# Optimization experiments

Measured on AMD Instinct MI355X. Metric: run time of the kernel, lower is better.

Reference implementation:

```python
import jax, jax.numpy as jnp
import numpy as np

# BERT-base dims
B, S = 32, 512
L, H, DH, DB, DFF, V = 12, 12, 64, 768, 3072, 30522
# Mamba2 dims
DM = 512            # d_model
DST = 128           # d_state
P = 64              # headdim
DI = 1024           # d_inner = expand * d_model
NH = DI // P        # 16 mamba heads
DCONV = 4
CONV_DIM = DI + 2 * DST
DIP = 2 * DI + 2 * DST + NH   # in_proj output width
ED = 256            # final embed_dim


def setup_inputs():
    keys = iter(jax.random.split(jax.random.key(0), 64))
    def nrm(shape, s=0.02):
        return jax.random.normal(next(keys), shape, jnp.float32) * s
    return {
        "input_ids": jax.random.randint(next(keys), (B, S), 0, V, jnp.int32),
        "attention_mask": jnp.ones((B, S), jnp.int32),
        # frozen BERT params (layer dims stacked on axis 0)
        "tok_emb": nrm((V, DB)), "pos_emb": nrm((S, DB)), "type_emb": nrm((2, DB)),
        "emb_ln_g": jnp.ones((DB,)), "emb_ln_b": jnp.zeros((DB,)),
        "Wq": nrm((L, DB, DB)), "bq": jnp.zeros((L, DB)),
        "Wk": nrm((L, DB, DB)), "bk": jnp.zeros((L, DB)),
        "Wv": nrm((L, DB, DB)), "bv": jnp.zeros((L, DB)),
        "Wo": nrm((L, DB, DB)), "bo": jnp.zeros((L, DB)),
        "ln1_g": jnp.ones((L, DB)), "ln1_b": jnp.zeros((L, DB)),
        "Wf1": nrm((L, DB, DFF)), "bf1": jnp.zeros((L, DFF)),
        "Wf2": nrm((L, DFF, DB)), "bf2": jnp.zeros((L, DB)),
        "ln2_g": jnp.ones((L, DB)), "ln2_b": jnp.zeros((L, DB)),
        # trainable head params
        "W_pb": nrm((DB, DM)), "b_pb": jnp.zeros((DM,)),
        "W_in": nrm((DM, DIP)),
        "conv_w": nrm((CONV_DIM, DCONV), 0.2), "conv_b": jnp.zeros((CONV_DIM,)),
        "dt_bias": nrm((NH,), 0.5),
        "A_log": jnp.log(jnp.arange(1, NH + 1, dtype=jnp.float32)),
        "Dskip": jnp.ones((NH,)),
        "norm_g": jnp.ones((DI,)),
        "W_out": nrm((DI, DM)),
        "W_proj": nrm((DM, ED)), "b_proj": jnp.zeros((ED,)),
    }


def _layernorm(x, g, b, eps=1e-12):
    m = x.mean(-1, keepdims=True)
    v = ((x - m) ** 2).mean(-1, keepdims=True)
    return (x - m) * jax.lax.rsqrt(v + eps) * g + b


def _bert(input_ids, attention_mask, p):
    x = p["tok_emb"][input_ids] + p["pos_emb"][None] + p["type_emb"][0]
    x = _layernorm(x, p["emb_ln_g"], p["emb_ln_b"])
    bias = jnp.where(attention_mask[:, None, None, :] > 0, 0.0, -1e9)  # [B,1,1,S]
    inv_sqrt_dh = 1.0 / np.sqrt(DH).astype(np.float32)

    def layer(x, w):
        Wq, bq, Wk, bk, Wv, bv, Wo, bo, g1, b1, W1, c1, W2, c2, g2, b2 = w
        q = (x @ Wq + bq).reshape(B, S, H, DH)
        k = (x @ Wk + bk).reshape(B, S, H, DH)
        v = (x @ Wv + bv).reshape(B, S, H, DH)
        sc = jnp.einsum("bqhd,bkhd->bhqk", q, k) * inv_sqrt_dh + bias
        a = jax.nn.softmax(sc, axis=-1)
        o = jnp.einsum("bhqk,bkhd->bqhd", a, v).reshape(B, S, DB) @ Wo + bo
        x = _layernorm(x + o, g1, b1)
        f = jax.nn.gelu(x @ W1 + c1) @ W2 + c2
        x = _layernorm(x + f, g2, b2)
        return x, None

    stacked = (p["Wq"], p["bq"], p["Wk"], p["bk"], p["Wv"], p["bv"], p["Wo"], p["bo"],
               p["ln1_g"], p["ln1_b"], p["Wf1"], p["bf1"], p["Wf2"], p["bf2"],
               p["ln2_g"], p["ln2_b"])
    x, _ = jax.lax.scan(layer, x, stacked)
    return x


def _mamba_head(bert_out, p):
    xm = bert_out @ p["W_pb"] + p["b_pb"]                       # [B,S,DM]
    zxbcdt = xm @ p["W_in"]                                     # [B,S,DIP]
    z = zxbcdt[..., :DI]
    xBC = zxbcdt[..., DI:DI + CONV_DIM]
    dt = jax.nn.softplus(zxbcdt[..., DI + CONV_DIM:] + p["dt_bias"])  # [B,S,NH]
    # causal depthwise conv1d (kernel DCONV) + silu
    xc = jax.lax.conv_general_dilated(
        xBC.transpose(0, 2, 1), p["conv_w"][:, None, :], (1,), [(DCONV - 1, 0)],
        dimension_numbers=("NCH", "OIH", "NCH"), feature_group_count=CONV_DIM)
    xBC = jax.nn.silu((xc + p["conv_b"][:, None]).transpose(0, 2, 1))
    xs = xBC[..., :DI].reshape(B, S, NH, P)
    Bm = xBC[..., DI:DI + DST]                                  # [B,S,N] (ngroups=1)
    Cm = xBC[..., DI + DST:]                                    # [B,S,N]
    A = -jnp.exp(p["A_log"])                                    # [NH]
    dA = jnp.exp(dt * A)                                        # [B,S,NH]
    dtx = dt[..., None] * xs                                    # [B,S,NH,P]

    def step(h, ins):                                           # h: [B,NH,P,N]
        dA_t, dtx_t, B_t, C_t = ins
        h = dA_t[:, :, None, None] * h + dtx_t[..., None] * B_t[:, None, None, :]
        y = jnp.einsum("bhpn,bn->bhp", h, C_t)
        return h, y

    h0 = jnp.zeros((B, NH, P, DST))
    _, y = jax.lax.scan(step, h0, (dA.transpose(1, 0, 2), dtx.transpose(1, 0, 2, 3),
                                   Bm.transpose(1, 0, 2), Cm.transpose(1, 0, 2)))
    y = y.transpose(1, 0, 2, 3) + p["Dskip"][None, None, :, None] * xs  # [B,S,NH,P]
    # gated RMSNorm: rmsnorm(y * silu(z)) * g
    y = y.reshape(B, S, DI) * jax.nn.silu(z)
    y = y * jax.lax.rsqrt((y * y).mean(-1, keepdims=True) + 1e-5) * p["norm_g"]
    out = y @ p["W_out"]                                        # [B,S,DM]
    pooled = out.mean(axis=1)                                   # [B,DM]
    return pooled @ p["W_proj"] + p["b_proj"]                   # [B,ED]


def reference(input_ids, attention_mask, tok_emb, pos_emb, type_emb, emb_ln_g, emb_ln_b,
              Wq, bq, Wk, bk, Wv, bv, Wo, bo, ln1_g, ln1_b, Wf1, bf1, Wf2, bf2, ln2_g, ln2_b,
              W_pb, b_pb, W_in, conv_w, conv_b, dt_bias, A_log, Dskip, norm_g, W_out,
              W_proj, b_proj):
    p = dict(locals())
    bert_out = _bert(input_ids, attention_mask, p)
    return _mamba_head(bert_out, p)
```

## Files before the change

### kernel.cpp

```cpp
#include <hip/hip_runtime.h>
#include <hip/hip_bf16.h>


typedef __attribute__((ext_vector_type(4))) float f32x4;
typedef __attribute__((ext_vector_type(4))) short s16x4;
typedef __attribute__((ext_vector_type(8))) short s16x8;

#define DEV __device__ __forceinline__

DEV short f2bf(float f) {
  union { float f; unsigned u; } x; x.f = f;
  unsigned r = x.u + 0x7fffu + ((x.u >> 16) & 1u);
  return (short)(r >> 16);
}
DEV float bf2f(short h) {
  union { unsigned u; float f; } x; x.u = ((unsigned)(unsigned short)h) << 16;
  return x.f;
}
DEV float gelu_f(float x) {
  float u = 0.7978845608028654f * (x + 0.044715f * x * x * x);
  return 0.5f * x * (1.f + tanhf(u));
}
DEV float silu_f(float x) { return x / (1.f + __expf(-x)); }

DEV void glds16(const short* g, short* l) {
  __builtin_amdgcn_global_load_lds(
      (const __attribute__((address_space(1))) void*)g,
      (__attribute__((address_space(3))) void*)l, 16, 0, 0);
}
DEV void glds16f(const float* g, float* l) {
  __builtin_amdgcn_global_load_lds(
      (const __attribute__((address_space(1))) void*)g,
      (__attribute__((address_space(3))) void*)l, 16, 0, 0);
}
DEV void glds4f(const float* g, float* l) {
  __builtin_amdgcn_global_load_lds(
      (const __attribute__((address_space(1))) void*)g,
      (__attribute__((address_space(3))) void*)l, 4, 0, 0);
}

DEV float block_reduce_sum_256(float v, float* red) {
  #pragma unroll
  for (int o = 1; o < 64; o <<= 1) v += __shfl_xor(v, o);
  __syncthreads();
  if ((threadIdx.x & 63) == 0) red[threadIdx.x >> 6] = v;
  __syncthreads();
  return red[0] + red[1] + red[2] + red[3];
}

DEV float wave_reduce_sum(float v) {
  #pragma unroll
  for (int o = 1; o < 64; o <<= 1) v += __shfl_xor(v, o);
  return v;
}

__global__ __launch_bounds__(256) void transconv4_all_kernel(
    const float* __restrict__ Wq, const float* __restrict__ Wk,
    const float* __restrict__ Wv, const float* __restrict__ Wo,
    short* __restrict__ Wall)
{
  int l = blockIdx.z >> 2, which = blockIdx.z & 3;
  const float* Wb = (which == 0) ? Wq : (which == 1) ? Wk : (which == 2) ? Wv : Wo;
  const float* W = Wb + (size_t)l * 589824;
  short* Wtz = Wall + (size_t)l * 7077888 + (size_t)which * 589824;
  __shared__ float tile[32][33];
  int tx = threadIdx.x & 31, ty = threadIdx.x >> 5;
  int n0 = blockIdx.x * 32, k0 = blockIdx.y * 32;
  #pragma unroll
  for (int i = 0; i < 4; i++)
    tile[ty + i * 8][tx] = W[(size_t)(k0 + ty + i * 8) * 768 + n0 + tx];
  __syncthreads();
  #pragma unroll
  for (int i = 0; i < 4; i++)
    Wtz[(size_t)(n0 + ty + i * 8) * 768 + k0 + tx] = f2bf(tile[tx][ty + i * 8]);
}

__global__ __launch_bounds__(256) void transconv_f1_all_kernel(
    const float* __restrict__ Wf1, short* __restrict__ Wall)
{
  int l = blockIdx.z;
  const float* W = Wf1 + (size_t)l * 2359296;
  short* Wt = Wall + (size_t)l * 7077888 + 2359296;
  __shared__ float tile[32][33];
  int tx = threadIdx.x & 31, ty = threadIdx.x >> 5;
  int n0 = blockIdx.x * 32, k0 = blockIdx.y * 32;
  #pragma unroll
  for (int i = 0; i < 4; i++)
    tile[ty + i * 8][tx] = W[(size_t)(k0 + ty + i * 8) * 3072 + n0 + tx];
  __syncthreads();
  #pragma unroll
  for (int i = 0; i < 4; i++)
    Wt[(size_t)(n0 + ty + i * 8) * 768 + k0 + tx] = f2bf(tile[tx][ty + i * 8]);
}

__global__ __launch_bounds__(256) void transconv_f2_all_kernel(
    const float* __restrict__ Wf2, short* __restrict__ Wall)
{
  int l = blockIdx.z;
  const float* W = Wf2 + (size_t)l * 2359296;
  short* Wt = Wall + (size_t)l * 7077888 + 4718592;
  __shared__ float tile[32][33];
  int tx = threadIdx.x & 31, ty = threadIdx.x >> 5;
  int n0 = blockIdx.x * 32, k0 = blockIdx.y * 32;
  #pragma unroll
  for (int i = 0; i < 4; i++)
    tile[ty + i * 8][tx] = W[(size_t)(k0 + ty + i * 8) * 768 + n0 + tx];
  __syncthreads();
  #pragma unroll
  for (int i = 0; i < 4; i++)
    Wt[(size_t)(n0 + ty + i * 8) * 3072 + k0 + tx] = f2bf(tile[tx][ty + i * 8]);
}

__global__ __launch_bounds__(256) void transconv_kernel(
    const float* __restrict__ W, short* __restrict__ Wt,
    int K, int N, int Npad)
{
  __shared__ float tile[32][33];
  int tx = threadIdx.x & 31, ty = threadIdx.x >> 5;
  int n0 = blockIdx.x * 32, k0 = blockIdx.y * 32;
  #pragma unroll
  for (int i = 0; i < 4; i++) {
    int k = k0 + ty + i * 8, n = n0 + tx;
    tile[ty + i * 8][tx] = (k < K && n < N) ? W[(size_t)k * N + n] : 0.f;
  }
  __syncthreads();
  #pragma unroll
  for (int i = 0; i < 4; i++) {
    int n = n0 + ty + i * 8, k = k0 + tx;
    if (n < Npad && k < K)
      Wt[(size_t)n * K + k] = f2bf(tile[tx][ty + i * 8]);
  }
}

__global__ void concatbias_all_kernel(const float* __restrict__ bq,
                                      const float* __restrict__ bk,
                                      const float* __restrict__ bv,
                                      float* __restrict__ cb)
{
  int i = blockIdx.x * 256 + threadIdx.x;
  if (i >= 12 * 2304) return;
  int l = i / 2304, c = i - l * 2304;
  cb[i] = (c < 768) ? bq[l * 768 + c]
        : (c < 1536) ? bk[l * 768 + c - 768] : bv[l * 768 + c - 1536];
}

template<int OUTMODE, int WN, int BM>
__global__ __launch_bounds__(512) void gemm3(
    const short* __restrict__ A, const short* __restrict__ Bt,
    const float* __restrict__ bias, short* __restrict__ Cout,
    int M, int N, int K)
{
  constexpr int BN = 64 * WN;
  constexpr int MI = (BM * WN) / 128;
  constexpr int WROWS = 16 * MI;
  constexpr int VMC = BM / 64 + BN / 64;
  __shared__ short As[2][BM * 64];
  __shared__ short Bs[2][BN * 64];
  const int t = threadIdx.x;
  const int lane = t & 63;
  const int lr = lane & 15, lg = lane >> 4;
  const int wid = t >> 6;
  const int wr = (WN == 4) ? (wid >> 2) : (wid >> 1);
  const int wc = (WN == 4) ? (wid & 3) : (wid & 1);

  const int nwg = gridDim.x * gridDim.y;
  const int lid = blockIdx.y * gridDim.x + blockIdx.x;
  const int xcd = lid & 7, rest = lid >> 3;
  const int qq = nwg >> 3, rr = nwg & 7;
  const int wgid = (xcd < rr ? xcd * (qq + 1) : rr * (qq + 1) + (xcd - rr) * qq) + rest;
  const int m0 = (wgid / gridDim.x) * BM;
  const int n0 = (wgid % gridDim.x) * BN;

  const short* Ab = A + (size_t)m0 * K;
  const short* Bb = Bt + (size_t)n0 * K;

  auto stage = [&](int buf, int k0) {
    #pragma unroll
    for (int i = 0; i < BM / 64; i++) {
      int idx = t + 512 * i;
      int row = idx >> 3, c = idx & 7;
      int cs = c ^ (row & 7);
      glds16(Ab + (size_t)row * K + k0 + cs * 8, &As[buf][idx * 8]);
    }
    #pragma unroll
    for (int i = 0; i < BN / 64; i++) {
      int idx = t + 512 * i;
      int row = idx >> 3, c = idx & 7;
      int cs = c ^ (row & 7);
      glds16(Bb + (size_t)row * K + k0 + cs * 8, &Bs[buf][idx * 8]);
    }
  };

  f32x4 acc[MI][4] = {};
  const int nt = K >> 6;

  stage(0, 0);
  stage(1, 64);

  for (int tt = 0; tt < nt; ++tt) {
    const int cur = tt & 1;
    if (tt + 1 < nt) {
      if constexpr (VMC == 8)      asm volatile("s_waitcnt vmcnt(8)" ::: "memory");
      else if constexpr (VMC == 6) asm volatile("s_waitcnt vmcnt(6)" ::: "memory");
      else                         asm volatile("s_waitcnt vmcnt(4)" ::: "memory");
    } else {
      asm volatile("s_waitcnt vmcnt(0)" ::: "memory");
    }
    __builtin_amdgcn_s_barrier();
    asm volatile("" ::: "memory");
    __builtin_amdgcn_sched_barrier(0);

    s16x8 af[MI][2], bfr[4][2];
    #pragma unroll
    for (int mi = 0; mi < MI; mi++) {
      int row = wr * WROWS + mi * 16 + lr;
      #pragma unroll
      for (int ks = 0; ks < 2; ks++) {
        int ck = (ks * 4 + lg) ^ (lr & 7);
        af[mi][ks] = *(const s16x8*)&As[cur][row * 64 + ck * 8];
      }
    }
    #pragma unroll
    for (int ni = 0; ni < 4; ni++) {
      int row = wc * 64 + ni * 16 + lr;
      #pragma unroll
      for (int ks = 0; ks < 2; ks++) {
        int ck = (ks * 4 + lg) ^ (lr & 7);
        bfr[ni][ks] = *(const s16x8*)&Bs[cur][row * 64 + ck * 8];
      }
    }
    asm volatile("s_waitcnt lgkmcnt(0)" ::: "memory");
    __builtin_amdgcn_sched_barrier(0);
    __builtin_amdgcn_s_barrier();
    asm volatile("" ::: "memory");
    __builtin_amdgcn_sched_barrier(0);

    if (tt + 2 < nt) stage(cur, (tt + 2) * 64);

    __builtin_amdgcn_s_setprio(1);
    #pragma unroll
    for (int ks = 0; ks < 2; ks++)
      #pragma unroll
      for (int mi = 0; mi < MI; mi++)
        #pragma unroll
        for (int ni = 0; ni < 4; ni++)
          acc[mi][ni] = __builtin_amdgcn_mfma_f32_16x16x32_bf16(
              af[mi][ks], bfr[ni][ks], acc[mi][ni], 0, 0, 0);
    __builtin_amdgcn_s_setprio(0);
  }

  #pragma unroll
  for (int mi = 0; mi < MI; mi++) {
    int row = m0 + wr * WROWS + mi * 16 + lg * 4;
    #pragma unroll
    for (int ni = 0; ni < 4; ni++) {
      int col = n0 + wc * 64 + ni * 16 + lr;
      if (col >= N) continue;
      float bv = bias ? bias[col] : 0.f;
      #pragma unroll
      for (int r = 0; r < 4; r++) {
        float v = acc[mi][ni][r] + bv;
        if (OUTMODE == 2) v = gelu_f(v);
        Cout[(size_t)(row + r) * N + col] = f2bf(v);
      }
    }
  }
}

template<int OUTMODE>
__global__ __launch_bounds__(256) void gemm2(
    const short* __restrict__ A, const short* __restrict__ Bt,
    const float* __restrict__ bias, void* __restrict__ Cout,
    int M, int N, int K)
{
  __shared__ short As[128 * 64];
  __shared__ short Bs[128 * 64];
  const int t = threadIdx.x;
  const int lane = t & 63;
  const int lr = lane & 15, lg = lane >> 4;
  const int wid = t >> 6, wm = wid >> 1, wn = wid & 1;

  const int nwg = gridDim.x * gridDim.y;
  const int lid = blockIdx.y * gridDim.x + blockIdx.x;
  const int xcd = lid & 7, rest = lid >> 3;
  const int qq = nwg >> 3, rr = nwg & 7;
  const int wgid = (xcd < rr ? xcd * (qq + 1) : rr * (qq + 1) + (xcd - rr) * qq) + rest;
  const int m0 = (wgid / gridDim.x) * 128;
  const int n0 = (wgid % gridDim.x) * 128;

  f32x4 acc[4][4] = {};
  const short* Ab = A + (size_t)m0 * K;
  const short* Bb = Bt + (size_t)n0 * K;

  for (int k0 = 0; k0 < K; k0 += 64) {
    __syncthreads();
    #pragma unroll
    for (int i = 0; i < 4; i++) {
      int idx = t + 256 * i;
      int row = idx >> 3, c = idx & 7;
      glds16(Ab + (size_t)row * K + k0 + c * 8, &As[idx * 8]);
    }
    #pragma unroll
    for (int i = 0; i < 4; i++) {
      int idx = t + 256 * i;
      int row = idx >> 3, c = idx & 7;
      glds16(Bb + (size_t)row * K + k0 + c * 8, &Bs[idx * 8]);
    }
    __syncthreads();
    #pragma unroll
    for (int ks = 0; ks < 2; ks++) {
      s16x8 af[4], bfr[4];
      #pragma unroll
      for (int mi = 0; mi < 4; mi++)
        af[mi] = *(const s16x8*)&As[(wm * 64 + mi * 16 + lr) * 64 + ks * 32 + lg * 8];
      #pragma unroll
      for (int ni = 0; ni < 4; ni++)
        bfr[ni] = *(const s16x8*)&Bs[(wn * 64 + ni * 16 + lr) * 64 + ks * 32 + lg * 8];
      #pragma unroll
      for (int mi = 0; mi < 4; mi++)
        #pragma unroll
        for (int ni = 0; ni < 4; ni++)
          acc[mi][ni] = __builtin_amdgcn_mfma_f32_16x16x32_bf16(
              af[mi], bfr[ni], acc[mi][ni], 0, 0, 0);
    }
  }

  #pragma unroll
  for (int mi = 0; mi < 4; mi++) {
    int row = m0 + wm * 64 + mi * 16 + lg * 4;
    #pragma unroll
    for (int ni = 0; ni < 4; ni++) {
      int col = n0 + wn * 64 + ni * 16 + lr;
      if (col >= N) continue;
      float bv = bias ? bias[col] : 0.f;
      #pragma unroll
      for (int r = 0; r < 4; r++) {
        float v = acc[mi][ni][r] + bv;
        if (OUTMODE == 2) v = gelu_f(v);
        size_t off = (size_t)(row + r) * N + col;
        if (OUTMODE == 0) ((float*)Cout)[off] = v;
        else              ((short*)Cout)[off] = f2bf(v);
      }
    }
  }
}

#define LDQ 2304
__global__ __launch_bounds__(512) void attn_kernel(
    const short* __restrict__ QKV, const float* __restrict__ biasv,
    short* __restrict__ O)
{
  __shared__ short Ks[64 * 72];
  __shared__ short Vt[64 * 68];
  __shared__ float bsh[64];
  const int t = threadIdx.x;
  const int lane = t & 63, wid = t >> 6;
  const int lr = lane & 15, lg = lane >> 4;
  const int b = blockIdx.z, h = blockIdx.y, q0 = blockIdx.x * 128;
  const float scale = 0.125f;

  s16x8 qf8[2];
  {
    const short* qp = QKV + (size_t)(b * 512 + q0 + wid * 16 + lr) * LDQ + h * 64;
    qf8[0] = *(const s16x8*)(qp + lg * 8);
    qf8[1] = *(const s16x8*)(qp + 32 + lg * 8);
  }

  f32x4 ot[4] = {};
  float lrun = 0.f;

  for (int kv0 = 0; kv0 < 512; kv0 += 64) {
    __syncthreads();
    {
      int row = t >> 3, c8 = (t & 7) * 8;
      *(s16x8*)&Ks[row * 72 + c8] =
          *(const s16x8*)(QKV + (size_t)(b * 512 + kv0 + row) * LDQ + 768 + h * 64 + c8);
    }
    {
      int kk = t & 63, dh = t >> 6;
      const short* vp = QKV + (size_t)(b * 512 + kv0 + kk) * LDQ + 1536 + h * 64 + dh * 8;
      s16x8 v0 = *(const s16x8*)vp;
      #pragma unroll
      for (int i = 0; i < 8; i++) Vt[(dh * 8 + i) * 68 + kk] = v0[i];
    }
    if (t < 64) bsh[t] = biasv[b * 512 + kv0 + t];
    __syncthreads();

    f32x4 st[4] = {};
    #pragma unroll
    for (int ks = 0; ks < 2; ks++) {
      #pragma unroll
      for (int a = 0; a < 4; a++) {
        s16x8 kf = *(const s16x8*)&Ks[(a * 16 + lr) * 72 + ks * 32 + lg * 8];
        st[a] = __builtin_amdgcn_mfma_f32_16x16x32_bf16(kf, qf8[ks], st[a], 0, 0, 0);
      }
    }
    float p[16];
    float rsum = 0.f;
    #pragma unroll
    for (int a = 0; a < 4; a++)
      #pragma unroll
      for (int r = 0; r < 4; r++) {
        float v = __expf(st[a][r] * scale + bsh[a * 16 + lg * 4 + r]);
        p[a * 4 + r] = v;
        rsum += v;
      }
    rsum += __shfl_xor(rsum, 16);
    rsum += __shfl_xor(rsum, 32);
    lrun += rsum;
    s16x4 ptf[4];
    #pragma unroll
    for (int ks = 0; ks < 4; ks++) {
      s16x4 f;
      #pragma unroll
      for (int j = 0; j < 4; j++) f[j] = f2bf(p[ks * 4 + j]);
      ptf[ks] = f;
    }
    #pragma unroll
    for (int ks = 0; ks < 4; ks++) {
      #pragma unroll
      for (int d = 0; d < 4; d++) {
        s16x4 vf = *(const s16x4*)&Vt[(d * 16 + lr) * 68 + ks * 16 + lg * 4];
        ot[d] = __builtin_amdgcn_mfma_f32_16x16x16bf16_1k(vf, ptf[ks], ot[d], 0, 0, 0);
      }
    }
  }

  float inv = 1.f / lrun;
  short* op = O + (size_t)(b * 512 + q0 + wid * 16 + lr) * 768 + h * 64;
  #pragma unroll
  for (int d = 0; d < 4; d++) {
    s16x4 w;
    #pragma unroll
    for (int r = 0; r < 4; r++) w[r] = f2bf(ot[d][r] * inv);
    *(s16x4*)(op + d * 16 + lg * 4) = w;
  }
}

__global__ void maskbias_kernel(const int* __restrict__ mask, float* __restrict__ biasv) {
  int i = blockIdx.x * 256 + threadIdx.x;
  if (i < 32 * 512) biasv[i] = mask[i] > 0 ? -8.0f : -1e9f;
}

__global__ __launch_bounds__(256) void embed_ln_kernel(
    const int* __restrict__ ids, const float* __restrict__ tok,
    const float* __restrict__ pos, const float* __restrict__ typ,
    const float* __restrict__ g, const float* __restrict__ bta,
    short* __restrict__ xb)
{
  __shared__ float red[4];
  int row = blockIdx.x, s = row & 511, t = threadIdx.x;
  int id = ids[row];
  float v[3], sum = 0.f;
  #pragma unroll
  for (int i = 0; i < 3; i++) {
    int c = t + 256 * i;
    float e = tok[(size_t)id * 768 + c] + pos[s * 768 + c] + typ[c];
    v[i] = e; sum += e;
  }
  float mean = block_reduce_sum_256(sum, red) * (1.f / 768.f);
  float var = 0.f;
  #pragma unroll
  for (int i = 0; i < 3; i++) { float d = v[i] - mean; var += d * d; }
  var = block_reduce_sum_256(var, red) * (1.f / 768.f);
  float rstd = rsqrtf(var + 1e-12f);
  #pragma unroll
  for (int i = 0; i < 3; i++) {
    int c = t + 256 * i;
    float o = (v[i] - mean) * rstd * g[c] + bta[c];
    xb[(size_t)row * 768 + c] = f2bf(o);
  }
}

__global__ __launch_bounds__(256) void add_ln_kernel(
    short* __restrict__ xb, const short* __restrict__ delta,
    const float* __restrict__ g, const float* __restrict__ bta)
{
  const int t = threadIdx.x;
  const int lane = t & 63, w = t >> 6;
  const int row = blockIdx.x * 4 + w;
  short* xp = xb + (size_t)row * 768;
  const short* dp = delta + (size_t)row * 768;

  float e[12];
  float sum = 0.f;
  #pragma unroll
  for (int i = 0; i < 3; i++) {
    int c4 = (lane + 64 * i) * 4;
    s16x4 xv = *(const s16x4*)(xp + c4);
    s16x4 dv = *(const s16x4*)(dp + c4);
    #pragma unroll
    for (int j = 0; j < 4; j++) {
      float v = bf2f(xv[j]) + bf2f(dv[j]);
      e[i * 4 + j] = v; sum += v;
    }
  }
  float mean = wave_reduce_sum(sum) * (1.f / 768.f);
  float var = 0.f;
  #pragma unroll
  for (int i = 0; i < 12; i++) { float d = e[i] - mean; var += d * d; }
  var = wave_reduce_sum(var) * (1.f / 768.f);
  float rstd = rsqrtf(var + 1e-12f);
  #pragma unroll
  for (int i = 0; i < 3; i++) {
    int c4 = (lane + 64 * i) * 4;
    f32x4 gv = *(const f32x4*)(g + c4);
    f32x4 bv = *(const f32x4*)(bta + c4);
    s16x4 o;
    #pragma unroll
    for (int j = 0; j < 4; j++)
      o[j] = f2bf((e[i * 4 + j] - mean) * rstd * gv[j] + bv[j]);
    *(s16x4*)(xp + c4) = o;
  }
}

__global__ void dtda_kernel(const short* __restrict__ zx,
                            const float* __restrict__ dt_bias,
                            const float* __restrict__ A_log,
                            float* __restrict__ dt, float* __restrict__ dA)
{
  int i = blockIdx.x * 256 + threadIdx.x;
  if (i >= 16384 * 16) return;
  int row = i >> 4, h = i & 15;
  float x = bf2f(zx[(size_t)row * 2320 + 2304 + h]) + dt_bias[h];
  float sp = (x > 20.f) ? x : log1pf(__expf(x));
  float a = -__expf(A_log[h]);
  dt[i] = sp;
  dA[i] = __expf(sp * a);
}

__global__ __launch_bounds__(256) void conv2_kernel(
    const short* __restrict__ zx, const float* __restrict__ cw,
    const float* __restrict__ cb, float* __restrict__ xc)
{
  int gid = blockIdx.x * 256 + threadIdx.x;
  int row = gid / 160, cg = gid - row * 160;
  if (row >= 16384) return;
  int s = row & 511, c0 = cg * 8;
  float acc[8];
  #pragma unroll
  for (int j = 0; j < 8; j++) acc[j] = cb[c0 + j];
  #pragma unroll
  for (int k = 0; k < 4; k++) {
    int sp = s - 3 + k;
    if (sp < 0) continue;
    s16x8 v = *(const s16x8*)&zx[(size_t)(row - 3 + k) * 2320 + 1024 + c0];
    #pragma unroll
    for (int j = 0; j < 8; j++) acc[j] += bf2f(v[j]) * cw[(c0 + j) * 4 + k];
  }
  #pragma unroll
  for (int j = 0; j < 8; j++)
    xc[(size_t)row * 1280 + c0 + j] = silu_f(acc[j]);
}

__global__ __launch_bounds__(256) void scan_kernel(
    const float* __restrict__ dt, const float* __restrict__ dA,
    const float* __restrict__ xc, float* __restrict__ y)
{
  __shared__ float sdA[512];
  __shared__ float sdt[512];
  __shared__ float sBC[2][4096];
  __shared__ float sX[2][1024];
  const int b = blockIdx.x >> 4, h = blockIdx.x & 15;
  const int t = threadIdx.x;
  const int p4 = t >> 4, nc = t & 15;
  const float* xcb = xc + (size_t)(b * 512) * 1280;

  const int st_s = t >> 6;
  const int ck   = t & 63;
  const int sck  = ck ^ ((ck >> 3) & 1);
  const int a0 = nc * 2,      pa0 = (a0 ^ ((a0 >> 3) & 1)) * 4;
  const int a1 = nc * 2 + 1,  pa1 = (a1 ^ ((a1 >> 3) & 1)) * 4;
  const int a2 = nc * 2 + 32, pa2 = (a2 ^ ((a2 >> 3) & 1)) * 4;
  const int a3 = nc * 2 + 33, pa3 = (a3 ^ ((a3 >> 3) & 1)) * 4;

  sdA[t] = dA[(b * 512 + t) * 16 + h];
  sdA[t + 256] = dA[(b * 512 + t + 256) * 16 + h];
  sdt[t] = dt[(b * 512 + t) * 16 + h];
  sdt[t + 256] = dt[(b * 512 + t + 256) * 16 + h];
  #pragma unroll
  for (int i = 0; i < 4; i++) {
    glds16f(xcb + (size_t)(st_s + 4 * i) * 1280 + 1024 + sck * 4, &sBC[0][(t + 256 * i) * 4]);
    glds4f (xcb + (size_t)(st_s + 4 * i) * 1280 + h * 64 + ck,    &sX[0][t + 256 * i]);
  }
  __syncthreads();

  float hA[8] = {0,0,0,0,0,0,0,0}, hB[8] = {0,0,0,0,0,0,0,0};
  float hC[8] = {0,0,0,0,0,0,0,0}, hD[8] = {0,0,0,0,0,0,0,0};
  float* yb0 = y + (size_t)(b * 512) * 1024 + h * 64;

  for (int c = 0; c < 32; ++c) {
    const int cur = c & 1;
    if (c < 31) {
      const float* src = xcb + (size_t)((c + 1) * 16) * 1280;
      #pragma unroll
      for (int i = 0; i < 4; i++) {
        glds16f(src + (size_t)(st_s + 4 * i) * 1280 + 1024 + sck * 4, &sBC[cur ^ 1][(t + 256 * i) * 4]);
        glds4f (src + (size_t)(st_s + 4 * i) * 1280 + h * 64 + ck,    &sX[cur ^ 1][t + 256 * i]);
      }
    }
    const float* bc = sBC[cur];
    const float* sx = sX[cur];
    const int sg0 = c * 16;
    #pragma unroll 2
    for (int st = 0; st < 16; ++st) {
      float dA0 = sdA[sg0 + st];
      float dt0 = sdt[sg0 + st];
      float xA = sx[st * 64 + p4];
      float xB = sx[st * 64 + p4 + 16];
      float xC = sx[st * 64 + p4 + 32];
      float xD = sx[st * 64 + p4 + 48];
      const float* base = bc + st * 256;
      f32x4 b0 = *(const f32x4*)(base + pa0);
      f32x4 b1 = *(const f32x4*)(base + pa1);
      f32x4 c0 = *(const f32x4*)(base + pa2);
      f32x4 c1 = *(const f32x4*)(base + pa3);
      float cxA = dt0 * xA, cxB = dt0 * xB, cxC = dt0 * xC, cxD = dt0 * xD;
      float psA = 0.f, psB = 0.f, psC = 0.f, psD = 0.f;
      #pragma unroll
      for (int j = 0; j < 4; j++) {
        hA[j] = dA0 * hA[j] + cxA * b0[j];  psA += hA[j] * c0[j];
        hB[j] = dA0 * hB[j] + cxB * b0[j];  psB += hB[j] * c0[j];
        hC[j] = dA0 * hC[j] + cxC * b0[j];  psC += hC[j] * c0[j];
        hD[j] = dA0 * hD[j] + cxD * b0[j];  psD += hD[j] * c0[j];
      }
      #pragma unroll
      for (int j = 0; j < 4; j++) {
        hA[4+j] = dA0 * hA[4+j] + cxA * b1[j];  psA += hA[4+j] * c1[j];
        hB[4+j] = dA0 * hB[4+j] + cxB * b1[j];  psB += hB[4+j] * c1[j];
        hC[4+j] = dA0 * hC[4+j] + cxC * b1[j];  psC += hC[4+j] * c1[j];
        hD[4+j] = dA0 * hD[4+j] + cxD * b1[j];  psD += hD[4+j] * c1[j];
      }
      psA += __shfl_xor(psA, 1); psB += __shfl_xor(psB, 1);
      psC += __shfl_xor(psC, 1); psD += __shfl_xor(psD, 1);
      psA += __shfl_xor(psA, 2); psB += __shfl_xor(psB, 2);
      psC += __shfl_xor(psC, 2); psD += __shfl_xor(psD, 2);
      psA += __shfl_xor(psA, 4); psB += __shfl_xor(psB, 4);
      psC += __shfl_xor(psC, 4); psD += __shfl_xor(psD, 4);
      psA += __shfl_xor(psA, 8); psB += __shfl_xor(psB, 8);
      psC += __shfl_xor(psC, 8); psD += __shfl_xor(psD, 8);
      if (nc == 0) {
        float* yr = yb0 + (size_t)(sg0 + st) * 1024;
        yr[p4]      = psA;
        yr[p4 + 16] = psB;
        yr[p4 + 32] = psC;
        yr[p4 + 48] = psD;
      }
    }
    __syncthreads();
  }
}

__global__ __launch_bounds__(256) void ycombine_kernel(
    const float* __restrict__ y, const float* __restrict__ xc,
    const short* __restrict__ zx, const float* __restrict__ Dskip,
    const float* __restrict__ norm_g, short* __restrict__ ybf)
{
  const int t = threadIdx.x;
  const int lane = t & 63, w = t >> 6;
  const int row = blockIdx.x * 4 + w;
  const float* yp = y + (size_t)row * 1024;
  const float* xp = xc + (size_t)row * 1280;
  const short* zp = zx + (size_t)row * 2320;

  float o[16];
  float ss = 0.f;
  #pragma unroll
  for (int i = 0; i < 4; i++) {
    int c = lane + 64 * i;
    int c4 = c * 4;
    f32x4 yv = *(const f32x4*)(yp + c4);
    f32x4 xv = *(const f32x4*)(xp + c4);
    s16x4 zv = *(const s16x4*)(zp + c4);
    float dsk = Dskip[c >> 4];
    #pragma unroll
    for (int j = 0; j < 4; j++) {
      float v = (yv[j] + dsk * xv[j]) * silu_f(bf2f(zv[j]));
      o[i * 4 + j] = v; ss += v * v;
    }
  }
  ss = wave_reduce_sum(ss) * (1.f / 1024.f);
  float rs = rsqrtf(ss + 1e-5f);
  #pragma unroll
  for (int i = 0; i < 4; i++) {
    int c4 = (lane + 64 * i) * 4;
    f32x4 gv = *(const f32x4*)(norm_g + c4);
    s16x4 ov;
    #pragma unroll
    for (int j = 0; j < 4; j++) ov[j] = f2bf(o[i * 4 + j] * rs * gv[j]);
    *(s16x4*)(ybf + (size_t)row * 1024 + c4) = ov;
  }
}

__global__ void pool2_kernel(const float* __restrict__ outb, float* __restrict__ part)
{
  int b = blockIdx.x, ch = blockIdx.y, d = threadIdx.x;
  const float* p = outb + ((size_t)(b * 512 + ch * 64)) * 512 + d;
  float s = 0.f;
  #pragma unroll 8
  for (int i = 0; i < 64; i++) s += p[(size_t)i * 512];
  part[(b * 8 + ch) * 512 + d] = s;
}

__global__ void poolred_kernel(const float* __restrict__ part, float* __restrict__ pooled)
{
  int b = blockIdx.x, d = threadIdx.x;
  float s = 0.f;
  #pragma unroll
  for (int c = 0; c < 8; c++) s += part[(b * 8 + c) * 512 + d];
  pooled[b * 512 + d] = s * (1.f / 512.f);
}

__global__ void finalproj_kernel(const float* __restrict__ pooled,
                                 const float* __restrict__ Wp,
                                 const float* __restrict__ bp,
                                 float* __restrict__ out)
{
  int b = blockIdx.x, n = threadIdx.x;
  float acc = bp[n];
  for (int k = 0; k < 512; k++) acc += pooled[b * 512 + k] * Wp[k * 256 + n];
  out[b * 256 + n] = acc;
}

extern "C" void kernel_launch(void* const* d_in, const int* in_sizes, int n_in,
                              void* d_out, int out_size, void* d_ws, size_t ws_size,
                              hipStream_t stream)
{
  const int*   ids      = (const int*)d_in[0];
  const int*   amask    = (const int*)d_in[1];
  const float* tok_emb  = (const float*)d_in[2];
  const float* pos_emb  = (const float*)d_in[3];
  const float* type_emb = (const float*)d_in[4];
  const float* emb_g    = (const float*)d_in[5];
  const float* emb_b    = (const float*)d_in[6];
  const float* Wq = (const float*)d_in[7];   const float* bq = (const float*)d_in[8];
  const float* Wk = (const float*)d_in[9];   const float* bk = (const float*)d_in[10];
  const float* Wv = (const float*)d_in[11];  const float* bv = (const float*)d_in[12];
  const float* Wo = (const float*)d_in[13];  const float* bo = (const float*)d_in[14];
  const float* ln1g = (const float*)d_in[15]; const float* ln1b = (const float*)d_in[16];
  const float* Wf1 = (const float*)d_in[17]; const float* bf1 = (const float*)d_in[18];
  const float* Wf2 = (const float*)d_in[19]; const float* bf2 = (const float*)d_in[20];
  const float* ln2g = (const float*)d_in[21]; const float* ln2b = (const float*)d_in[22];
  const float* W_pb = (const float*)d_in[23]; const float* b_pb = (const float*)d_in[24];
  const float* W_in = (const float*)d_in[25];
  const float* conv_w = (const float*)d_in[26]; const float* conv_b = (const float*)d_in[27];
  const float* dt_bias = (const float*)d_in[28]; const float* A_log = (const float*)d_in[29];
  const float* Dskip = (const float*)d_in[30]; const float* norm_g = (const float*)d_in[31];
  const float* W_out = (const float*)d_in[32];
  const float* W_proj = (const float*)d_in[33]; const float* b_proj = (const float*)d_in[34];

  char* base = (char*)d_ws;
  const size_t o_xb   = 0;
  const size_t o_wall = 25165824;
  const size_t o_bv   = o_wall + 169869312;
  const size_t o_cb   = o_bv + 65536;
  const size_t o_gtb  = o_cb + 131072;
  const size_t o_qkv  = o_gtb + 25165824;
  const size_t o_ao   = o_qkv + 75497472;
  const size_t o_ff   = o_ao + 25165824;
  const size_t bert_end = o_ff + 100663296;
  const size_t o_hw  = o_wall;
  const size_t o_xm  = o_hw + 4325376;
  const size_t o_zx  = o_xm + 16777216;
  const size_t o_xc  = o_zx + 76021760;
  const size_t o_dt  = o_xc + 83886080;
  const size_t o_dA  = o_dt + 1048576;
  const size_t o_y   = o_dA + 1048576;
  const size_t o_ybf = o_y  + 67108864;
  const size_t o_ob  = o_ybf + 33554432;
  const size_t o_pl  = o_ob + 33554432;
  const size_t o_pp  = o_pl + 65536;
  const size_t head_end = o_pp + 524288;
  const size_t need = (head_end > bert_end ? head_end : bert_end);
  if (ws_size < need) return;

  short* xb   = (short*)(base + o_xb);
  short* wall = (short*)(base + o_wall);
  float* bvp  = (float*)(base + o_bv);
  float* cbia = (float*)(base + o_cb);
  short* gtb  = (short*)(base + o_gtb);
  short* qkvb = (short*)(base + o_qkv);
  short* aob  = (short*)(base + o_ao);
  short* ffb  = (short*)(base + o_ff);
  short* hw   = (short*)(base + o_hw);
  short* xm   = (short*)(base + o_xm);
  short* zx   = (short*)(base + o_zx);
  float* xc   = (float*)(base + o_xc);
  float* dtb  = (float*)(base + o_dt);
  float* dAb  = (float*)(base + o_dA);
  float* yb   = (float*)(base + o_y);
  short* ybf  = (short*)(base + o_ybf);
  float* ob   = (float*)(base + o_ob);
  float* pl   = (float*)(base + o_pl);
  float* pp   = (float*)(base + o_pp);

  short* w_pbt  = hw;
  short* w_int  = w_pbt + 393216;
  short* w_outt = w_int + 1245184;

  const int M = 16384;
  dim3 blk(256);

  transconv4_all_kernel<<<dim3(24, 24, 48), blk, 0, stream>>>(Wq, Wk, Wv, Wo, wall);
  transconv_f1_all_kernel<<<dim3(96, 24, 12), blk, 0, stream>>>(Wf1, wall);
  transconv_f2_all_kernel<<<dim3(24, 96, 12), blk, 0, stream>>>(Wf2, wall);
  concatbias_all_kernel<<<108, 256, 0, stream>>>(bq, bk, bv, cbia);

  maskbias_kernel<<<64, 256, 0, stream>>>(amask, bvp);
  embed_ln_kernel<<<16384, 256, 0, stream>>>(ids, tok_emb, pos_emb, type_emb,
                                             emb_g, emb_b, xb);

  for (int l = 0; l < 12; l++) {
    short* wl = wall + (size_t)l * 7077888;
    gemm3<1, 2, 128><<<dim3(18, 128), 512, 0, stream>>>(xb, wl, cbia + l * 2304, qkvb, M, 2304, 768);
    attn_kernel<<<dim3(4, 12, 32), 512, 0, stream>>>(qkvb, bvp, aob);
    gemm3<1, 2, 128><<<dim3(6, 128), 512, 0, stream>>>(aob, wl + 3ull * 589824, bo + l * 768, gtb, M, 768, 768);
    add_ln_kernel<<<4096, 256, 0, stream>>>(xb, gtb, ln1g + l * 768, ln1b + l * 768);
    gemm3<2, 2, 128><<<dim3(24, 128), 512, 0, stream>>>(xb, wl + 2359296, bf1 + l * 3072, ffb, M, 3072, 768);
    gemm3<1, 2, 128><<<dim3(6, 128), 512, 0, stream>>>(ffb, wl + 4718592, bf2 + l * 768, gtb, M, 768, 3072);
    add_ln_kernel<<<4096, 256, 0, stream>>>(xb, gtb, ln2g + l * 768, ln2b + l * 768);
  }

  transconv_kernel<<<dim3(16, 24), blk, 0, stream>>>(W_pb, w_pbt, 768, 512, 512);
  gemm3<1, 2, 128><<<dim3(4, 128), 512, 0, stream>>>(xb, w_pbt, b_pb, xm, M, 512, 768);
  transconv_kernel<<<dim3(76, 16), blk, 0, stream>>>(W_in, w_int, 512, 2320, 2432);
  gemm3<1, 2, 128><<<dim3(19, 128), 512, 0, stream>>>(xm, w_int, nullptr, zx, M, 2320, 512);
  dtda_kernel<<<1024, 256, 0, stream>>>(zx, dt_bias, A_log, dtb, dAb);
  conv2_kernel<<<10240, 256, 0, stream>>>(zx, conv_w, conv_b, xc);
  scan_kernel<<<512, 256, 0, stream>>>(dtb, dAb, xc, yb);
  ycombine_kernel<<<4096, 256, 0, stream>>>(yb, xc, zx, Dskip, norm_g, ybf);
  transconv_kernel<<<dim3(16, 32), blk, 0, stream>>>(W_out, w_outt, 1024, 512, 512);
  gemm2<0><<<dim3(4, 128), blk, 0, stream>>>(ybf, w_outt, nullptr, ob, M, 512, 1024);
  pool2_kernel<<<dim3(32, 8), 512, 0, stream>>>(ob, pp);
  poolred_kernel<<<32, 512, 0, stream>>>(pp, pl);
  finalproj_kernel<<<32, 256, 0, stream>>>(pl, W_proj, b_proj, (float*)d_out);
}
```

Before: 5.594 ms.

## Split scan headdim across two blocks and halve chunk size

```diff
diff --git a/kernel.cpp b/kernel.cpp
--- a/kernel.cpp
+++ b/kernel.cpp
@@ -559,16 +559,18 @@
 {
   __shared__ float sdA[512];
   __shared__ float sdt[512];
-  __shared__ float sBC[2][4096];
-  __shared__ float sX[2][1024];
-  const int b = blockIdx.x >> 4, h = blockIdx.x & 15;
+  __shared__ float sBC[2][2048];
+  __shared__ float sX[2][512];
+  const int bx = blockIdx.x;
+  const int b = bx >> 5, h = (bx >> 1) & 15, psplit = bx & 1;
   const int t = threadIdx.x;
-  const int p4 = t >> 4, nc = t & 15;
+  const int pr = t >> 4, nc = t & 15;
+  const int pgA = psplit * 32 + pr;
+  const int pgB = pgA + 16;
   const float* xcb = xc + (size_t)(b * 512) * 1280;
 
-  const int st_s = t >> 6;
-  const int ck   = t & 63;
-  const int sck  = ck ^ ((ck >> 3) & 1);
+  const int ck  = t & 63;
+  const int sck = ck ^ ((ck >> 3) & 1);
   const int a0 = nc * 2,      pa0 = (a0 ^ ((a0 >> 3) & 1)) * 4;
   const int a1 = nc * 2 + 1,  pa1 = (a1 ^ ((a1 >> 3) & 1)) * 4;
   const int a2 = nc * 2 + 32, pa2 = (a2 ^ ((a2 >> 3) & 1)) * 4;
@@ -579,72 +581,63 @@
   sdt[t] = dt[(b * 512 + t) * 16 + h];
   sdt[t + 256] = dt[(b * 512 + t + 256) * 16 + h];
   #pragma unroll
-  for (int i = 0; i < 4; i++) {
-    glds16f(xcb + (size_t)(st_s + 4 * i) * 1280 + 1024 + sck * 4, &sBC[0][(t + 256 * i) * 4]);
-    glds4f (xcb + (size_t)(st_s + 4 * i) * 1280 + h * 64 + ck,    &sX[0][t + 256 * i]);
+  for (int i = 0; i < 2; i++) {
+    int idx = t + 256 * i;
+    int row = idx >> 6;
+    glds16f(xcb + (size_t)row * 1280 + 1024 + sck * 4, &sBC[0][idx * 4]);
+    glds4f (xcb + (size_t)row * 1280 + h * 64 + ck,    &sX[0][idx]);
   }
   __syncthreads();
 
   float hA[8] = {0,0,0,0,0,0,0,0}, hB[8] = {0,0,0,0,0,0,0,0};
-  float hC[8] = {0,0,0,0,0,0,0,0}, hD[8] = {0,0,0,0,0,0,0,0};
   float* yb0 = y + (size_t)(b * 512) * 1024 + h * 64;
 
-  for (int c = 0; c < 32; ++c) {
+  for (int c = 0; c < 64; ++c) {
     const int cur = c & 1;
-    if (c < 31) {
-      const float* src = xcb + (size_t)((c + 1) * 16) * 1280;
-      #pragma unroll
-      for (int i = 0; i < 4; i++) {
-        glds16f(src + (size_t)(st_s + 4 * i) * 1280 + 1024 + sck * 4, &sBC[cur ^ 1][(t + 256 * i) * 4]);
-        glds4f (src + (size_t)(st_s + 4 * i) * 1280 + h * 64 + ck,    &sX[cur ^ 1][t + 256 * i]);
+    if (c < 63) {
+      const float* src = xcb + (size_t)((c + 1) * 8) * 1280;
+      #pragma unroll
+      for (int i = 0; i < 2; i++) {
+        int idx = t + 256 * i;
+        int row = idx >> 6;
+        glds16f(src + (size_t)row * 1280 + 1024 + sck * 4, &sBC[cur ^ 1][idx * 4]);
+        glds4f (src + (size_t)row * 1280 + h * 64 + ck,    &sX[cur ^ 1][idx]);
       }
     }
     const float* bc = sBC[cur];
     const float* sx = sX[cur];
-    const int sg0 = c * 16;
+    const int sg0 = c * 8;
     #pragma unroll 2
-    for (int st = 0; st < 16; ++st) {
+    for (int st = 0; st < 8; ++st) {
       float dA0 = sdA[sg0 + st];
       float dt0 = sdt[sg0 + st];
-      float xA = sx[st * 64 + p4];
-      float xB = sx[st * 64 + p4 + 16];
-      float xC = sx[st * 64 + p4 + 32];
-      float xD = sx[st * 64 + p4 + 48];
+      float xA = sx[st * 64 + pgA];
+      float xB = sx[st * 64 + pgB];
       const float* base = bc + st * 256;
       f32x4 b0 = *(const f32x4*)(base + pa0);
       f32x4 b1 = *(const f32x4*)(base + pa1);
       f32x4 c0 = *(const f32x4*)(base + pa2);
       f32x4 c1 = *(const f32x4*)(base + pa3);
-      float cxA = dt0 * xA, cxB = dt0 * xB, cxC = dt0 * xC, cxD = dt0 * xD;
-      float psA = 0.f, psB = 0.f, psC = 0.f, psD = 0.f;
+      float cxA = dt0 * xA, cxB = dt0 * xB;
+      float psA = 0.f, psB = 0.f;
       #pragma unroll
       for (int j = 0; j < 4; j++) {
         hA[j] = dA0 * hA[j] + cxA * b0[j];  psA += hA[j] * c0[j];
         hB[j] = dA0 * hB[j] + cxB * b0[j];  psB += hB[j] * c0[j];
-        hC[j] = dA0 * hC[j] + cxC * b0[j];  psC += hC[j] * c0[j];
-        hD[j] = dA0 * hD[j] + cxD * b0[j];  psD += hD[j] * c0[j];
       }
       #pragma unroll
       for (int j = 0; j < 4; j++) {
         hA[4+j] = dA0 * hA[4+j] + cxA * b1[j];  psA += hA[4+j] * c1[j];
         hB[4+j] = dA0 * hB[4+j] + cxB * b1[j];  psB += hB[4+j] * c1[j];
-        hC[4+j] = dA0 * hC[4+j] + cxC * b1[j];  psC += hC[4+j] * c1[j];
-        hD[4+j] = dA0 * hD[4+j] + cxD * b1[j];  psD += hD[4+j] * c1[j];
       }
       psA += __shfl_xor(psA, 1); psB += __shfl_xor(psB, 1);
-      psC += __shfl_xor(psC, 1); psD += __shfl_xor(psD, 1);
       psA += __shfl_xor(psA, 2); psB += __shfl_xor(psB, 2);
-      psC += __shfl_xor(psC, 2); psD += __shfl_xor(psD, 2);
       psA += __shfl_xor(psA, 4); psB += __shfl_xor(psB, 4);
-      psC += __shfl_xor(psC, 4); psD += __shfl_xor(psD, 4);
       psA += __shfl_xor(psA, 8); psB += __shfl_xor(psB, 8);
-      psC += __shfl_xor(psC, 8); psD += __shfl_xor(psD, 8);
       if (nc == 0) {
         float* yr = yb0 + (size_t)(sg0 + st) * 1024;
-        yr[p4]      = psA;
-        yr[p4 + 16] = psB;
-        yr[p4 + 32] = psC;
-        yr[p4 + 48] = psD;
+        yr[pgA] = psA;
+        yr[pgB] = psB;
       }
     }
     __syncthreads();
@@ -827,7 +820,7 @@
   gemm3<1, 2, 128><<<dim3(19, 128), 512, 0, stream>>>(xm, w_int, nullptr, zx, M, 2320, 512);
   dtda_kernel<<<1024, 256, 0, stream>>>(zx, dt_bias, A_log, dtb, dAb);
   conv2_kernel<<<10240, 256, 0, stream>>>(zx, conv_w, conv_b, xc);
-  scan_kernel<<<512, 256, 0, stream>>>(dtb, dAb, xc, yb);
+  scan_kernel<<<1024, 256, 0, stream>>>(dtb, dAb, xc, yb);
   ycombine_kernel<<<4096, 256, 0, stream>>>(yb, xc, zx, Dskip, norm_g, ybf);
   transconv_kernel<<<dim3(16, 32), blk, 0, stream>>>(W_out, w_outt, 1024, 512, 512);
   gemm2<0><<<dim3(4, 128), blk, 0, stream>>>(ybf, w_outt, nullptr, ob, M, 512, 1024);
```

Measured after the change: 5.617 ms. About the same (+0.4%).
